# Kernel optimization log

Hardware: AMD Instinct MI355X
Metric: run time of the kernel (lower is better)

## Reference

```python
import jax, jax.numpy as jnp
import numpy as np

HEADS = 12
ROPE_THETA = 10000.0

def _rope(t):
    # t: [B, H, N, D]; lucidrains interleaved RoPE (rotate_half over adjacent pairs)
    B, H, N, D = t.shape
    inv_freq = 1.0 / (ROPE_THETA ** (jnp.arange(0, D, 2, dtype=jnp.float32) / D))  # [D/2]
    freqs = jnp.arange(N, dtype=jnp.float32)[:, None] * inv_freq[None, :]          # [N, D/2]
    freqs = jnp.repeat(freqs, 2, axis=-1)                                          # [N, D]
    cos, sin = jnp.cos(freqs), jnp.sin(freqs)
    tp = t.reshape(B, H, N, D // 2, 2)
    rot = jnp.stack([-tp[..., 1], tp[..., 0]], axis=-1).reshape(B, H, N, D)
    return t * cos + rot * sin

def setup_inputs() -> dict:
    key = jax.random.key(0)
    k1, k2, k3 = jax.random.split(key, 3)
    dim = 768
    x = jax.random.normal(k1, (2, 2048, dim), dtype=jnp.float32)
    w_qkv = jax.random.normal(k2, (3 * dim, dim), dtype=jnp.float32) * (dim ** -0.5)
    w_proj = jax.random.normal(k3, (dim, dim), dtype=jnp.float32) * (dim ** -0.5)
    b_proj = jnp.zeros((dim,), dtype=jnp.float32)
    return {"x": x, "w_qkv": w_qkv, "w_proj": w_proj, "b_proj": b_proj}

def reference(x, w_qkv, w_proj, b_proj):
    B, N, C = x.shape
    H = HEADS
    d = C // H
    scale = d ** -0.5
    qkv = x @ w_qkv.T                                # [B, N, 3C]
    q, k, v = jnp.split(qkv, 3, axis=-1)
    def to_heads(t):
        return t.reshape(B, N, H, d).transpose(0, 2, 1, 3)  # [B,H,N,d]
    q, k, v = map(to_heads, (q, k, v))
    q = _rope(q * scale)
    k = _rope(k)
    attn = jnp.einsum('bhid,bhjd->bhij', q, k)
    attn = jax.nn.softmax(attn, axis=-1)
    out = jnp.einsum('bhij,bhjd->bhid', attn, v)
    out = out.transpose(0, 2, 1, 3).reshape(B, N, C)
    return out @ w_proj.T + b_proj
```

## Files before the change

kernel.cpp:

```cpp
#include <hip/hip_runtime.h>
#include <math.h>

#define NSEQ 2048
#define CDIM 768
#define NH   12
#define HD   64
#define NB   2

typedef unsigned short u16;
typedef __attribute__((ext_vector_type(8))) short bf16x8;
typedef __attribute__((ext_vector_type(4))) float f32x4;
typedef __attribute__((ext_vector_type(8))) float f32x8;
typedef __attribute__((ext_vector_type(4))) __bf16 bf16x4t;
typedef __attribute__((ext_vector_type(8))) __bf16 bf16x8t;

__device__ __forceinline__ u16 f2bf(float x) {
    unsigned int u = __float_as_uint(x);
    u += 0x7fffu + ((u >> 16) & 1u);
    return (u16)(u >> 16);
}

__device__ __forceinline__ uint4 pack8(float4 a, float4 b) {
    f32x8 v = {a.x, a.y, a.z, a.w, b.x, b.y, b.z, b.w};
    union { bf16x8t t; uint4 u; } o;
    o.t = __builtin_convertvector(v, bf16x8t);
    return o.u;
}

__device__ __forceinline__ float fexp2(float x) {
#if __has_builtin(__builtin_amdgcn_exp2f)
    return __builtin_amdgcn_exp2f(x);
#else
    float r; asm("v_exp_f32 %0, %1" : "=v"(r) : "v"(x)); return r;
#endif
}

#define LSTR 72
#define ESTR 136

#define GLD16(gp, lp) __builtin_amdgcn_global_load_lds( \
    (__attribute__((address_space(1))) void*)(const void*)(gp), \
    (__attribute__((address_space(3))) void*)(void*)(lp), 16, 0, 0)

__global__ __launch_bounds__(256)
void conv_kernel(const float* __restrict__ Xf, const float* __restrict__ Wqkv,
                 const float* __restrict__ Wproj, u16* __restrict__ Xb,
                 u16* __restrict__ Wqb, u16* __restrict__ Wpb)
{
    const int c = blockIdx.x * 256 + threadIdx.x;
    const float* src; u16* dst; int lc; float scl = 1.0f;
    if (c < 393216)      { src = Xf;    dst = Xb;  lc = c; }
    else if (c < 614400) { src = Wqkv;  dst = Wqb; lc = c - 393216;
                           if (lc < 73728) scl = 0.18033688011112042f; }
    else                 { src = Wproj; dst = Wpb; lc = c - 614400; }
    float4 a = *(const float4*)&src[(size_t)lc * 8];
    float4 b = *(const float4*)&src[(size_t)lc * 8 + 4];
    a.x *= scl; a.y *= scl; a.z *= scl; a.w *= scl;
    b.x *= scl; b.y *= scl; b.z *= scl; b.w *= scl;
    *(uint4*)&dst[(size_t)lc * 8] = pack8(a, b);
}

#define QKV_STAGE(BUF, kt_) do {                                              \
    _Pragma("unroll")                                                         \
    for (int it = 0; it < 4; ++it) {                                          \
        int ch = tid + 256 * it; int rr = ch >> 3;                            \
        int sc = ((ch & 7) ^ (rr & 7)) << 3;                                  \
        GLD16(Xg + (size_t)(m0 + rr) * CDIM + (kt_) + sc, &S[BUF][ch * 8]);   \
    }                                                                         \
    _Pragma("unroll")                                                         \
    for (int it = 0; it < 2; ++it) {                                          \
        int ch = tid + 256 * it; int rr = ch >> 3;                            \
        int sc = ((ch & 7) ^ (rr & 7)) << 3;                                  \
        GLD16(Wg + (size_t)(n0 + rr) * CDIM + (kt_) + sc,                     \
              &S[BUF][8192 + ch * 8]);                                        \
    }                                                                         \
} while (0)

__global__ __launch_bounds__(256)
void qkv_mfma_kernel(const u16* __restrict__ Xg, const u16* __restrict__ Wg,
                     u16* __restrict__ Qb, u16* __restrict__ Kb,
                     u16* __restrict__ Vb)
{
    __shared__ __align__(16) u16 S[2][12288];

    const int tid  = threadIdx.x;
    const int lane = tid & 63;
    const int wid  = tid >> 6;
    const int l15  = lane & 15;
    const int quad = lane >> 4;
    const int swz  = (l15 & 7) << 3;

    const int f  = blockIdx.x;
    const int xc = f & 7;
    const int s  = f >> 3;
    const int m0 = (xc * 4 + (s & 3)) * 128;
    const int n0 = (s >> 2) * 64;

    f32x4 acc[2][4];
#pragma unroll
    for (int mi = 0; mi < 2; ++mi)
#pragma unroll
        for (int ni = 0; ni < 4; ++ni)
            acc[mi][ni] = (f32x4){0.f, 0.f, 0.f, 0.f};

    QKV_STAGE(0, 0);
    __syncthreads();

    int cur = 0;
    for (int kt = 0; kt < CDIM; kt += 64) {
        if (kt + 64 < CDIM) QKV_STAGE(cur ^ 1, kt + 64);

#pragma unroll
        for (int k = 0; k < 2; ++k) {
            bf16x8 af[2];
#pragma unroll
            for (int mi = 0; mi < 2; ++mi)
                af[mi] = *(const bf16x8*)
                    &S[cur][(wid * 32 + mi * 16 + l15) * 64
                            + ((quad * 8 + 32 * k) ^ swz)];
#pragma unroll
            for (int ni = 0; ni < 4; ++ni) {
                bf16x8 bfr = *(const bf16x8*)
                    &S[cur][8192 + (ni * 16 + l15) * 64
                            + ((quad * 8 + 32 * k) ^ swz)];
#pragma unroll
                for (int mi = 0; mi < 2; ++mi)
                    acc[mi][ni] = __builtin_amdgcn_mfma_f32_16x16x32_bf16(
                        af[mi], bfr, acc[mi][ni], 0, 0, 0);
            }
        }
        __syncthreads();
        cur ^= 1;
    }

    const int bi      = m0 >> 11;
    const int tokbase = m0 & 2047;
    const int nbase   = tokbase + wid * 32;
    const int sel     = n0 / CDIM;
    const int h       = (n0 % CDIM) >> 6;
    u16* Sf = &S[0][0];

    if (sel == 2) {
        u16* Ew = Sf;
#pragma unroll
        for (int ni = 0; ni < 4; ++ni)
#pragma unroll
            for (int mi = 0; mi < 2; ++mi)
#pragma unroll
                for (int r = 0; r < 4; ++r)
                    Ew[(ni * 16 + l15) * ESTR + wid * 32 + mi * 16 + quad * 4 + r]
                        = f2bf(acc[mi][ni][r]);
        __syncthreads();
        u16* dst = Vb + (size_t)(bi * NH + h) * HD * NSEQ;
#pragma unroll
        for (int it = 0; it < 4; ++it) {
            int idx = tid + 256 * it;
            int dd  = idx >> 4;
            int c8  = (idx & 15) << 3;
            *(uint4*)&dst[(size_t)dd * NSEQ + tokbase + c8] =
                *(const uint4*)&Ew[dd * ESTR + c8];
        }
    } else {
        u16* dst = ((sel == 0) ? Qb : Kb) + (size_t)(bi * NH + h) * NSEQ * HD;
        u16* Ew = Sf + wid * 32 * LSTR;
#pragma unroll
        for (int ni = 0; ni < 4; ++ni) {
            int dd = ni * 16 + l15;
            float invf = expf(-0.14391156831212787f * (float)(dd & ~1));
#pragma unroll
            for (int mi = 0; mi < 2; ++mi) {
                f32x4 val = acc[mi][ni];
#pragma unroll
                for (int r = 0; r < 4; ++r) {
                    float e = val[r];
                    float p = __shfl_xor(e, 1);
                    int n = nbase + mi * 16 + quad * 4 + r;
                    float sv, cv;
                    __sincosf((float)n * invf, &sv, &cv);
                    float o = (dd & 1) ? (e * cv + p * sv)
                                       : (e * cv - p * sv);
                    Ew[(mi * 16 + quad * 4 + r) * LSTR + dd] = f2bf(o);
                }
            }
        }
#pragma unroll
        for (int it = 0; it < 4; ++it) {
            int ch  = lane + 64 * it;
            int tr  = ch >> 3;
            int gc8 = (ch & 7) << 3;
            *(uint4*)&dst[(size_t)(nbase + tr) * HD + gc8] =
                *(const uint4*)&Ew[tr * LSTR + gc8];
        }
    }
}

#define STAGE_KV(BUF, kt_) do {                                               \
    GLD16(Kg + ((size_t)(((kt_) << 6) + r0) * HD + cs),                       \
          &Ks[BUF][wid * 512]);                                               \
    GLD16(Kg + ((size_t)(((kt_) << 6) + r0 + 32) * HD + cs),                  \
          &Ks[BUF][wid * 512 + 2048]);                                        \
    GLD16(Vg + ((size_t)r0 * NSEQ + ((kt_) << 6) + cs),                       \
          &Vs[BUF][wid * 512]);                                               \
    GLD16(Vg + ((size_t)(r0 + 32) * NSEQ + ((kt_) << 6) + cs),                \
          &Vs[BUF][wid * 512 + 2048]);                                        \
} while (0)

#define ATTN_STEP(kt_, CUR, NXT) do {                                         \
    if ((kt_) + 1 < NSEQ / 64) STAGE_KV(NXT, (kt_) + 1);                      \
    f32x4 sacc[4];                                                            \
    _Pragma("unroll")                                                         \
    for (int mt = 0; mt < 4; ++mt) sacc[mt] = (f32x4){0.f, 0.f, 0.f, 0.f};    \
    __builtin_amdgcn_s_setprio(1);                                            \
    _Pragma("unroll")                                                         \
    for (int k = 0; k < 2; ++k) {                                             \
        _Pragma("unroll")                                                     \
        for (int mt = 0; mt < 4; ++mt) {                                      \
            bf16x8 ak = *(const bf16x8*)                                      \
                &Ks[CUR][(mt * 16 + l15) * 64 + ((quad * 8 + 32 * k) ^ swz)]; \
            sacc[mt] = __builtin_amdgcn_mfma_f32_16x16x32_bf16(               \
                ak, aq[k], sacc[mt], 0, 0, 0);                                \
        }                                                                     \
    }                                                                         \
    __builtin_amdgcn_s_setprio(0);                                            \
    _Pragma("unroll")                                                         \
    for (int mt = 0; mt < 4; ++mt) {                                          \
        f32x4 ev;                                                             \
        _Pragma("unroll")                                                     \
        for (int r = 0; r < 4; ++r) ev[r] = fexp2(sacc[mt][r]);               \
        bf16x4t pbk = __builtin_convertvector(ev, bf16x4t);                   \
        *(bf16x4t*)&Pw[l15 * 64 + ((mt * 16 + quad * 4) ^ swz)] = pbk;        \
    }                                                                         \
    __builtin_amdgcn_s_setprio(1);                                            \
    _Pragma("unroll")                                                         \
    for (int k = 0; k < 2; ++k) {                                             \
        bf16x8 ap = *(const bf16x8*)                                          \
            &Pw[l15 * 64 + ((quad * 8 + 32 * k) ^ swz)];                      \
        lacc = __builtin_amdgcn_mfma_f32_16x16x32_bf16(                       \
            ap, vone, lacc, 0, 0, 0);                                         \
        _Pragma("unroll")                                                     \
        for (int t = 0; t < 4; ++t) {                                         \
            bf16x8 bv = *(const bf16x8*)                                      \
                &Vs[CUR][(t * 16 + l15) * 64 + ((quad * 8 + 32 * k) ^ swz)];  \
            O[t] = __builtin_amdgcn_mfma_f32_16x16x32_bf16(                   \
                ap, bv, O[t], 0, 0, 0);                                       \
        }                                                                     \
    }                                                                         \
    __builtin_amdgcn_s_setprio(0);                                            \
    __syncthreads();                                                          \
} while (0)

__global__ __launch_bounds__(256)
void attn_kernel(const u16* __restrict__ Qb, const u16* __restrict__ Kb,
                 const u16* __restrict__ Vt, u16* __restrict__ AO)
{
    __shared__ __align__(16) u16 Ks[2][64 * 64];
    __shared__ __align__(16) u16 Vs[2][64 * 64];
    __shared__ __align__(16) u16 Ps[4][16 * 64];

    const int tid  = threadIdx.x;
    const int lane = tid & 63;
    const int wid  = tid >> 6;
    const int l15  = lane & 15;
    const int quad = lane >> 4;
    const int swz  = (l15 & 7) << 3;

    const int f  = blockIdx.x;
    const int i  = f >> 3;
    const int bh = (f & 7) * 3 + (i >> 5);
    const int qt = i & 31;

    const u16* Qg = Qb + ((size_t)bh * NSEQ + qt * 64) * HD;
    const u16* Kg = Kb + (size_t)bh * NSEQ * HD;
    const u16* Vg = Vt + (size_t)bh * HD * NSEQ;

    const int r0 = tid >> 3;
    const int cs = ((tid & 7) ^ (r0 & 7)) << 3;

    bf16x8 aq[2];
    aq[0] = *(const bf16x8*)&Qg[(wid * 16 + l15) * HD + quad * 8];
    aq[1] = *(const bf16x8*)&Qg[(wid * 16 + l15) * HD + quad * 8 + 32];

    union { u16 s[8]; bf16x8 v; } oneu;
#pragma unroll
    for (int ii = 0; ii < 8; ++ii) oneu.s[ii] = 0x3f80;
    const bf16x8 vone = oneu.v;

    f32x4 O[4];
#pragma unroll
    for (int t = 0; t < 4; ++t) O[t] = (f32x4){0.f, 0.f, 0.f, 0.f};
    f32x4 lacc = (f32x4){0.f, 0.f, 0.f, 0.f};

    u16* Pw = Ps[wid];

    STAGE_KV(0, 0);
    __syncthreads();

    for (int kt = 0; kt < NSEQ / 64; kt += 2) {
        ATTN_STEP(kt, 0, 1);
        ATTN_STEP(kt + 1, 1, 0);
    }

    float inv4[4];
#pragma unroll
    for (int r = 0; r < 4; ++r) inv4[r] = 1.0f / lacc[r];

    const int b = bh / NH, h = bh % NH;
#pragma unroll
    for (int r = 0; r < 4; ++r) {
        size_t orow = (size_t)b * NSEQ + qt * 64 + wid * 16 + quad * 4 + r;
#pragma unroll
        for (int t = 0; t < 4; ++t)
            AO[orow * CDIM + h * HD + t * 16 + l15] = f2bf(O[t][r] * inv4[r]);
    }
}

#define PROJ_STAGE(BUF, kt_) do {                                             \
    _Pragma("unroll")                                                         \
    for (int it = 0; it < 2; ++it) {                                          \
        int ch = tid + 256 * it; int rr = ch >> 3;                            \
        int sc = ((ch & 7) ^ (rr & 7)) << 3;                                  \
        GLD16(Ag + (size_t)(m0 + rr) * CDIM + (kt_) + sc, &S[BUF][ch * 8]);   \
        GLD16(Wg + (size_t)(n0 + rr) * CDIM + (kt_) + sc,                     \
              &S[BUF][4096 + ch * 8]);                                        \
    }                                                                         \
} while (0)

__global__ __launch_bounds__(256)
void proj_kernel(const u16* __restrict__ Ag, const u16* __restrict__ Wg,
                 const float* __restrict__ bias, float* __restrict__ out)
{
    __shared__ __align__(16) u16 S[2][8192];
    const int tid  = threadIdx.x;
    const int lane = tid & 63;
    const int wid  = tid >> 6;
    const int l15  = lane & 15;
    const int quad = lane >> 4;
    const int swz  = (l15 & 7) << 3;
    const int wr = wid >> 1, wc = wid & 1;

    const int f  = blockIdx.x;
    const int xc = f & 7;
    const int s  = f >> 3;
    const int m0 = (xc * 8 + (s & 7)) * 64;
    const int n0 = (s >> 3) * 64;

    f32x4 acc[2][2];
#pragma unroll
    for (int mi = 0; mi < 2; ++mi)
#pragma unroll
        for (int ni = 0; ni < 2; ++ni)
            acc[mi][ni] = (f32x4){0.f, 0.f, 0.f, 0.f};

    PROJ_STAGE(0, 0);
    __syncthreads();

    int cur = 0;
    for (int kt = 0; kt < CDIM; kt += 64) {
        if (kt + 64 < CDIM) PROJ_STAGE(cur ^ 1, kt + 64);

#pragma unroll
        for (int k = 0; k < 2; ++k) {
            bf16x8 af[2], bf[2];
#pragma unroll
            for (int mi = 0; mi < 2; ++mi)
                af[mi] = *(const bf16x8*)
                    &S[cur][(wr * 32 + mi * 16 + l15) * 64
                            + ((quad * 8 + 32 * k) ^ swz)];
#pragma unroll
            for (int ni = 0; ni < 2; ++ni)
                bf[ni] = *(const bf16x8*)
                    &S[cur][4096 + (wc * 32 + ni * 16 + l15) * 64
                            + ((quad * 8 + 32 * k) ^ swz)];
#pragma unroll
            for (int mi = 0; mi < 2; ++mi)
#pragma unroll
                for (int ni = 0; ni < 2; ++ni)
                    acc[mi][ni] = __builtin_amdgcn_mfma_f32_16x16x32_bf16(
                        af[mi], bf[ni], acc[mi][ni], 0, 0, 0);
        }
        __syncthreads();
        cur ^= 1;
    }

#pragma unroll
    for (int ni = 0; ni < 2; ++ni) {
        int col = n0 + wc * 32 + ni * 16 + l15;
        float bb = bias[col];
#pragma unroll
        for (int mi = 0; mi < 2; ++mi) {
            int rw = m0 + wr * 32 + mi * 16 + quad * 4;
#pragma unroll
            for (int r = 0; r < 4; ++r)
                out[(size_t)(rw + r) * CDIM + col] = acc[mi][ni][r] + bb;
        }
    }
}

extern "C" void kernel_launch(void* const* d_in, const int* in_sizes, int n_in,
                              void* d_out, int out_size, void* d_ws,
                              size_t ws_size, hipStream_t stream)
{
    const float* X     = (const float*)d_in[0];
    const float* Wqkv  = (const float*)d_in[1];
    const float* Wproj = (const float*)d_in[2];
    const float* bias  = (const float*)d_in[3];
    float* out = (float*)d_out;

    const size_t per_buf = (size_t)NB * NH * NSEQ * HD;
    u16* Qb  = (u16*)d_ws;
    u16* Kb  = Qb + per_buf;
    u16* Vb  = Kb + per_buf;
    u16* XAO = Vb + per_buf;
    u16* Wqb = XAO + per_buf;
    u16* Wpb = Wqb + (size_t)3 * CDIM * CDIM;

    conv_kernel<<<dim3(2688), 256, 0, stream>>>(X, Wqkv, Wproj, XAO, Wqb, Wpb);
    qkv_mfma_kernel<<<dim3(1152), 256, 0, stream>>>(XAO, Wqb, Qb, Kb, Vb);
    attn_kernel<<<dim3(768), 256, 0, stream>>>(Qb, Kb, Vb, XAO);
    proj_kernel<<<dim3(768), 256, 0, stream>>>(XAO, Wpb, bias, out);
}
```

Baseline: 144.8 us.

## Switch attention to 32x32x16 MFMA with split-KV warps and register-shuffled P

New measurement: 147.5 us. No clear change (+1.9%).

```diff
diff --git a/kernel.cpp b/kernel.cpp
--- a/kernel.cpp
+++ b/kernel.cpp
@@ -11,6 +11,9 @@
 typedef __attribute__((ext_vector_type(8))) short bf16x8;
 typedef __attribute__((ext_vector_type(4))) float f32x4;
 typedef __attribute__((ext_vector_type(8))) float f32x8;
+typedef __attribute__((ext_vector_type(16))) float f32x16;
+typedef __attribute__((ext_vector_type(2))) float f32x2;
+typedef __attribute__((ext_vector_type(2))) __bf16 bf16x2t;
 typedef __attribute__((ext_vector_type(4))) __bf16 bf16x4t;
 typedef __attribute__((ext_vector_type(8))) __bf16 bf16x8t;
 
@@ -24,6 +27,12 @@
     f32x8 v = {a.x, a.y, a.z, a.w, b.x, b.y, b.z, b.w};
     union { bf16x8t t; uint4 u; } o;
     o.t = __builtin_convertvector(v, bf16x8t);
+    return o.u;
+}
+
+__device__ __forceinline__ unsigned cvtpk(float lo, float hi) {
+    union { bf16x2t t; unsigned u; } o;
+    o.t = __builtin_convertvector((f32x2){lo, hi}, bf16x2t);
     return o.u;
 }
 
@@ -195,57 +204,55 @@
 }
 
 #define STAGE_KV(BUF, kt_) do {                                               \
-    GLD16(Kg + ((size_t)(((kt_) << 6) + r0) * HD + cs),                       \
-          &Ks[BUF][wid * 512]);                                               \
-    GLD16(Kg + ((size_t)(((kt_) << 6) + r0 + 32) * HD + cs),                  \
-          &Ks[BUF][wid * 512 + 2048]);                                        \
-    GLD16(Vg + ((size_t)r0 * NSEQ + ((kt_) << 6) + cs),                       \
-          &Vs[BUF][wid * 512]);                                               \
-    GLD16(Vg + ((size_t)(r0 + 32) * NSEQ + ((kt_) << 6) + cs),                \
-          &Vs[BUF][wid * 512 + 2048]);                                        \
+    _Pragma("unroll")                                                         \
+    for (int j_ = 0; j_ < 2; ++j_) {                                          \
+        int c0_ = wid * 128 + j_ * 64;                                        \
+        int rr  = (c0_ + lane) >> 3;                                          \
+        int sc  = ((lane & 7) ^ (rr & 7)) << 3;                               \
+        GLD16(Kg + ((size_t)(((kt_) << 6) + rr) * HD + sc),                   \
+              &Ks[BUF][c0_ * 8]);                                             \
+        GLD16(Vg + ((size_t)rr * NSEQ + ((kt_) << 6) + sc),                   \
+              &Vs[BUF][c0_ * 8]);                                             \
+    }                                                                         \
 } while (0)
 
 #define ATTN_STEP(kt_, CUR, NXT) do {                                         \
     if ((kt_) + 1 < NSEQ / 64) STAGE_KV(NXT, (kt_) + 1);                      \
-    f32x4 sacc[4];                                                            \
-    _Pragma("unroll")                                                         \
-    for (int mt = 0; mt < 4; ++mt) sacc[mt] = (f32x4){0.f, 0.f, 0.f, 0.f};    \
+    f32x16 s0 = {};                                                           \
     __builtin_amdgcn_s_setprio(1);                                            \
     _Pragma("unroll")                                                         \
-    for (int k = 0; k < 2; ++k) {                                             \
-        _Pragma("unroll")                                                     \
-        for (int mt = 0; mt < 4; ++mt) {                                      \
-            bf16x8 ak = *(const bf16x8*)                                      \
-                &Ks[CUR][(mt * 16 + l15) * 64 + ((quad * 8 + 32 * k) ^ swz)]; \
-            sacc[mt] = __builtin_amdgcn_mfma_f32_16x16x32_bf16(               \
-                ak, aq[k], sacc[mt], 0, 0, 0);                                \
-        }                                                                     \
+    for (int s = 0; s < 4; ++s) {                                             \
+        bf16x8 ak = *(const bf16x8*)                                          \
+            &Ks[CUR][(wk * 32 + l31) * 64 + ((16 * s + 8 * hi) ^ swz)];       \
+        s0 = __builtin_amdgcn_mfma_f32_32x32x16_bf16(ak, bq[s], s0, 0, 0, 0); \
     }                                                                         \
     __builtin_amdgcn_s_setprio(0);                                            \
     _Pragma("unroll")                                                         \
-    for (int mt = 0; mt < 4; ++mt) {                                          \
-        f32x4 ev;                                                             \
-        _Pragma("unroll")                                                     \
-        for (int r = 0; r < 4; ++r) ev[r] = fexp2(sacc[mt][r]);               \
-        bf16x4t pbk = __builtin_convertvector(ev, bf16x4t);                   \
-        *(bf16x4t*)&Pw[l15 * 64 + ((mt * 16 + quad * 4) ^ swz)] = pbk;        \
-    }                                                                         \
-    __builtin_amdgcn_s_setprio(1);                                            \
-    _Pragma("unroll")                                                         \
-    for (int k = 0; k < 2; ++k) {                                             \
-        bf16x8 ap = *(const bf16x8*)                                          \
-            &Pw[l15 * 64 + ((quad * 8 + 32 * k) ^ swz)];                      \
-        lacc = __builtin_amdgcn_mfma_f32_16x16x32_bf16(                       \
-            ap, vone, lacc, 0, 0, 0);                                         \
-        _Pragma("unroll")                                                     \
-        for (int t = 0; t < 4; ++t) {                                         \
-            bf16x8 bv = *(const bf16x8*)                                      \
-                &Vs[CUR][(t * 16 + l15) * 64 + ((quad * 8 + 32 * k) ^ swz)];  \
-            O[t] = __builtin_amdgcn_mfma_f32_16x16x32_bf16(                   \
-                ap, bv, O[t], 0, 0, 0);                                       \
-        }                                                                     \
-    }                                                                         \
-    __builtin_amdgcn_s_setprio(0);                                            \
+    for (int r = 0; r < 16; ++r) s0[r] = fexp2(s0[r]);                        \
+    _Pragma("unroll")                                                         \
+    for (int t = 0; t < 2; ++t) {                                             \
+        const int sl = 8 * t;                                                 \
+        unsigned w0 = cvtpk(s0[sl + 0], s0[sl + 1]);                          \
+        unsigned w1 = cvtpk(s0[sl + 2], s0[sl + 3]);                          \
+        unsigned w2 = cvtpk(s0[sl + 4], s0[sl + 5]);                          \
+        unsigned w3 = cvtpk(s0[sl + 6], s0[sl + 7]);                          \
+        unsigned x0 = (unsigned)__shfl_xor((int)w0, 32);                      \
+        unsigned x1 = (unsigned)__shfl_xor((int)w1, 32);                      \
+        unsigned x2 = (unsigned)__shfl_xor((int)w2, 32);                      \
+        unsigned x3 = (unsigned)__shfl_xor((int)w3, 32);                      \
+        union { unsigned w[4]; bf16x8 v; } ap;                                \
+        ap.w[0] = hi ? x2 : w0;  ap.w[1] = hi ? x3 : w1;                      \
+        ap.w[2] = hi ? w2 : x0;  ap.w[3] = hi ? w3 : x1;                      \
+        const int vc = (wk * 32 + 16 * t + 8 * hi) ^ swz;                     \
+        bf16x8 bv0 = *(const bf16x8*)&Vs[CUR][l31 * 64 + vc];                 \
+        bf16x8 bv1 = *(const bf16x8*)&Vs[CUR][(32 + l31) * 64 + vc];          \
+        __builtin_amdgcn_s_setprio(1);                                        \
+        lacc = __builtin_amdgcn_mfma_f32_32x32x16_bf16(ap.v, vone, lacc,      \
+                                                       0, 0, 0);              \
+        O0 = __builtin_amdgcn_mfma_f32_32x32x16_bf16(ap.v, bv0, O0, 0, 0, 0); \
+        O1 = __builtin_amdgcn_mfma_f32_32x32x16_bf16(ap.v, bv1, O1, 0, 0, 0); \
+        __builtin_amdgcn_s_setprio(0);                                        \
+    }                                                                         \
     __syncthreads();                                                          \
 } while (0)
 
@@ -255,14 +262,15 @@
 {
     __shared__ __align__(16) u16 Ks[2][64 * 64];
     __shared__ __align__(16) u16 Vs[2][64 * 64];
-    __shared__ __align__(16) u16 Ps[4][16 * 64];
 
     const int tid  = threadIdx.x;
     const int lane = tid & 63;
     const int wid  = tid >> 6;
-    const int l15  = lane & 15;
-    const int quad = lane >> 4;
-    const int swz  = (l15 & 7) << 3;
+    const int wq   = wid >> 1;
+    const int wk   = wid & 1;
+    const int l31  = lane & 31;
+    const int hi   = lane >> 5;
+    const int swz  = (l31 & 7) << 3;
 
     const int f  = blockIdx.x;
     const int i  = f >> 3;
@@ -273,24 +281,18 @@
     const u16* Kg = Kb + (size_t)bh * NSEQ * HD;
     const u16* Vg = Vt + (size_t)bh * HD * NSEQ;
 
-    const int r0 = tid >> 3;
-    const int cs = ((tid & 7) ^ (r0 & 7)) << 3;
-
-    bf16x8 aq[2];
-    aq[0] = *(const bf16x8*)&Qg[(wid * 16 + l15) * HD + quad * 8];
-    aq[1] = *(const bf16x8*)&Qg[(wid * 16 + l15) * HD + quad * 8 + 32];
+    bf16x8 bq[4];
+#pragma unroll
+    for (int s = 0; s < 4; ++s)
+        bq[s] = *(const bf16x8*)&Qg[(wq * 32 + l31) * HD + 16 * s + 8 * hi];
 
     union { u16 s[8]; bf16x8 v; } oneu;
 #pragma unroll
     for (int ii = 0; ii < 8; ++ii) oneu.s[ii] = 0x3f80;
     const bf16x8 vone = oneu.v;
 
-    f32x4 O[4];
-#pragma unroll
-    for (int t = 0; t < 4; ++t) O[t] = (f32x4){0.f, 0.f, 0.f, 0.f};
-    f32x4 lacc = (f32x4){0.f, 0.f, 0.f, 0.f};
-
-    u16* Pw = Ps[wid];
+    f32x16 O0 = {}, O1 = {};
+    f32x16 lacc = {};
 
     STAGE_KV(0, 0);
     __syncthreads();
@@ -300,17 +302,33 @@
         ATTN_STEP(kt + 1, 1, 0);
     }
 
-    float inv4[4];
-#pragma unroll
-    for (int r = 0; r < 4; ++r) inv4[r] = 1.0f / lacc[r];
-
-    const int b = bh / NH, h = bh % NH;
-#pragma unroll
-    for (int r = 0; r < 4; ++r) {
-        size_t orow = (size_t)b * NSEQ + qt * 64 + wid * 16 + quad * 4 + r;
-#pragma unroll
-        for (int t = 0; t < 4; ++t)
-            AO[orow * CDIM + h * HD + t * 16 + l15] = f2bf(O[t][r] * inv4[r]);
+    float* CB = (wq == 0) ? (float*)&Ks[0][0] : (float*)&Vs[0][0];
+    if (wk == 1) {
+#pragma unroll
+        for (int r = 0; r < 16; ++r) {
+            CB[r * 64 + lane]        = O0[r];
+            CB[1024 + r * 64 + lane] = O1[r];
+            CB[2048 + r * 64 + lane] = lacc[r];
+        }
+    }
+    __syncthreads();
+    if (wk == 0) {
+#pragma unroll
+        for (int r = 0; r < 16; ++r) {
+            O0[r]   += CB[r * 64 + lane];
+            O1[r]   += CB[1024 + r * 64 + lane];
+            lacc[r] += CB[2048 + r * 64 + lane];
+        }
+        const int b = bh / NH, h = bh % NH;
+        const size_t base = ((size_t)b * NSEQ + qt * 64 + wq * 32) * CDIM
+                            + h * HD;
+#pragma unroll
+        for (int r = 0; r < 16; ++r) {
+            const int q = (r & 3) + 8 * (r >> 2) + 4 * hi;
+            const float iv = 1.0f / lacc[r];
+            AO[base + (size_t)q * CDIM + l31]      = f2bf(O0[r] * iv);
+            AO[base + (size_t)q * CDIM + 32 + l31] = f2bf(O1[r] * iv);
+        }
     }
 }
 
```

## Split attention waves into 2x2 query/key grid with cross-wave reduction

Applied to the files above, without the earlier changes.

Measured after the change: 158.2 us. 1.09x slower.

```diff
diff --git a/kernel.cpp b/kernel.cpp
--- a/kernel.cpp
+++ b/kernel.cpp
@@ -37,6 +37,7 @@
 
 #define LSTR 72
 #define ESTR 136
+#define PSTR 72
 
 #define GLD16(gp, lp) __builtin_amdgcn_global_load_lds( \
     (__attribute__((address_space(1))) void*)(const void*)(gp), \
@@ -207,42 +208,57 @@
 
 #define ATTN_STEP(kt_, CUR, NXT) do {                                         \
     if ((kt_) + 1 < NSEQ / 64) STAGE_KV(NXT, (kt_) + 1);                      \
-    f32x4 sacc[4];                                                            \
-    _Pragma("unroll")                                                         \
-    for (int mt = 0; mt < 4; ++mt) sacc[mt] = (f32x4){0.f, 0.f, 0.f, 0.f};    \
+    f32x4 sacc[2][2];                                                         \
+    _Pragma("unroll")                                                         \
+    for (int g = 0; g < 2; ++g)                                               \
+        _Pragma("unroll")                                                     \
+        for (int mt = 0; mt < 2; ++mt)                                        \
+            sacc[g][mt] = (f32x4){0.f, 0.f, 0.f, 0.f};                        \
     __builtin_amdgcn_s_setprio(1);                                            \
     _Pragma("unroll")                                                         \
     for (int k = 0; k < 2; ++k) {                                             \
         _Pragma("unroll")                                                     \
-        for (int mt = 0; mt < 4; ++mt) {                                      \
+        for (int mt = 0; mt < 2; ++mt) {                                      \
             bf16x8 ak = *(const bf16x8*)                                      \
-                &Ks[CUR][(mt * 16 + l15) * 64 + ((quad * 8 + 32 * k) ^ swz)]; \
-            sacc[mt] = __builtin_amdgcn_mfma_f32_16x16x32_bf16(               \
-                ak, aq[k], sacc[mt], 0, 0, 0);                                \
+                &Ks[CUR][(wk * 32 + mt * 16 + l15) * 64                       \
+                         + ((quad * 8 + 32 * k) ^ swz)];                      \
+            sacc[0][mt] = __builtin_amdgcn_mfma_f32_16x16x32_bf16(            \
+                ak, aq[0][k], sacc[0][mt], 0, 0, 0);                          \
+            sacc[1][mt] = __builtin_amdgcn_mfma_f32_16x16x32_bf16(            \
+                ak, aq[1][k], sacc[1][mt], 0, 0, 0);                          \
         }                                                                     \
     }                                                                         \
     __builtin_amdgcn_s_setprio(0);                                            \
     _Pragma("unroll")                                                         \
-    for (int mt = 0; mt < 4; ++mt) {                                          \
-        f32x4 ev;                                                             \
+    for (int g = 0; g < 2; ++g)                                               \
         _Pragma("unroll")                                                     \
-        for (int r = 0; r < 4; ++r) ev[r] = fexp2(sacc[mt][r]);               \
-        bf16x4t pbk = __builtin_convertvector(ev, bf16x4t);                   \
-        *(bf16x4t*)&Pw[l15 * 64 + ((mt * 16 + quad * 4) ^ swz)] = pbk;        \
-    }                                                                         \
+        for (int mt = 0; mt < 2; ++mt) {                                      \
+            f32x4 ev;                                                         \
+            _Pragma("unroll")                                                 \
+            for (int r = 0; r < 4; ++r) ev[r] = fexp2(sacc[g][mt][r]);        \
+            bf16x4t pbk = __builtin_convertvector(ev, bf16x4t);               \
+            *(bf16x4t*)&Pw[l15 * PSTR + g * 32                                \
+                           + ((mt * 16 + quad * 4) ^ pswz)] = pbk;            \
+        }                                                                     \
     __builtin_amdgcn_s_setprio(1);                                            \
-    _Pragma("unroll")                                                         \
-    for (int k = 0; k < 2; ++k) {                                             \
-        bf16x8 ap = *(const bf16x8*)                                          \
-            &Pw[l15 * 64 + ((quad * 8 + 32 * k) ^ swz)];                      \
-        lacc = __builtin_amdgcn_mfma_f32_16x16x32_bf16(                       \
-            ap, vone, lacc, 0, 0, 0);                                         \
+    {                                                                         \
+        bf16x8 ap0 = *(const bf16x8*)                                         \
+            &Pw[l15 * PSTR + ((quad * 8) ^ pswz)];                            \
+        bf16x8 ap1 = *(const bf16x8*)                                         \
+            &Pw[l15 * PSTR + 32 + ((quad * 8) ^ pswz)];                       \
+        lacc[0] = __builtin_amdgcn_mfma_f32_16x16x32_bf16(                    \
+            ap0, vone, lacc[0], 0, 0, 0);                                     \
+        lacc[1] = __builtin_amdgcn_mfma_f32_16x16x32_bf16(                    \
+            ap1, vone, lacc[1], 0, 0, 0);                                     \
         _Pragma("unroll")                                                     \
         for (int t = 0; t < 4; ++t) {                                         \
             bf16x8 bv = *(const bf16x8*)                                      \
-                &Vs[CUR][(t * 16 + l15) * 64 + ((quad * 8 + 32 * k) ^ swz)];  \
-            O[t] = __builtin_amdgcn_mfma_f32_16x16x32_bf16(                   \
-                ap, bv, O[t], 0, 0, 0);                                       \
+                &Vs[CUR][(t * 16 + l15) * 64                                  \
+                         + ((wk * 32 + quad * 8) ^ swz)];                     \
+            O[0][t] = __builtin_amdgcn_mfma_f32_16x16x32_bf16(                \
+                ap0, bv, O[0][t], 0, 0, 0);                                   \
+            O[1][t] = __builtin_amdgcn_mfma_f32_16x16x32_bf16(                \
+                ap1, bv, O[1][t], 0, 0, 0);                                   \
         }                                                                     \
     }                                                                         \
     __builtin_amdgcn_s_setprio(0);                                            \
@@ -255,14 +271,17 @@
 {
     __shared__ __align__(16) u16 Ks[2][64 * 64];
     __shared__ __align__(16) u16 Vs[2][64 * 64];
-    __shared__ __align__(16) u16 Ps[4][16 * 64];
+    __shared__ __align__(16) u16 Ps[4][16 * PSTR];
 
     const int tid  = threadIdx.x;
     const int lane = tid & 63;
     const int wid  = tid >> 6;
+    const int wq   = wid >> 1;
+    const int wk   = wid & 1;
     const int l15  = lane & 15;
     const int quad = lane >> 4;
     const int swz  = (l15 & 7) << 3;
+    const int pswz = (l15 & 3) << 3;
 
     const int f  = blockIdx.x;
     const int i  = f >> 3;
@@ -276,19 +295,27 @@
     const int r0 = tid >> 3;
     const int cs = ((tid & 7) ^ (r0 & 7)) << 3;
 
-    bf16x8 aq[2];
-    aq[0] = *(const bf16x8*)&Qg[(wid * 16 + l15) * HD + quad * 8];
-    aq[1] = *(const bf16x8*)&Qg[(wid * 16 + l15) * HD + quad * 8 + 32];
+    bf16x8 aq[2][2];
+#pragma unroll
+    for (int g = 0; g < 2; ++g)
+#pragma unroll
+        for (int k = 0; k < 2; ++k)
+            aq[g][k] = *(const bf16x8*)
+                &Qg[(wq * 32 + g * 16 + l15) * HD + quad * 8 + 32 * k];
 
     union { u16 s[8]; bf16x8 v; } oneu;
 #pragma unroll
     for (int ii = 0; ii < 8; ++ii) oneu.s[ii] = 0x3f80;
     const bf16x8 vone = oneu.v;
 
-    f32x4 O[4];
-#pragma unroll
-    for (int t = 0; t < 4; ++t) O[t] = (f32x4){0.f, 0.f, 0.f, 0.f};
-    f32x4 lacc = (f32x4){0.f, 0.f, 0.f, 0.f};
+    f32x4 O[2][4];
+#pragma unroll
+    for (int g = 0; g < 2; ++g)
+#pragma unroll
+        for (int t = 0; t < 4; ++t) O[g][t] = (f32x4){0.f, 0.f, 0.f, 0.f};
+    f32x4 lacc[2];
+    lacc[0] = (f32x4){0.f, 0.f, 0.f, 0.f};
+    lacc[1] = (f32x4){0.f, 0.f, 0.f, 0.f};
 
     u16* Pw = Ps[wid];
 
@@ -300,17 +327,37 @@
         ATTN_STEP(kt + 1, 1, 0);
     }
 
-    float inv4[4];
-#pragma unroll
-    for (int r = 0; r < 4; ++r) inv4[r] = 1.0f / lacc[r];
-
-    const int b = bh / NH, h = bh % NH;
-#pragma unroll
-    for (int r = 0; r < 4; ++r) {
-        size_t orow = (size_t)b * NSEQ + qt * 64 + wid * 16 + quad * 4 + r;
-#pragma unroll
-        for (int t = 0; t < 4; ++t)
-            AO[orow * CDIM + h * HD + t * 16 + l15] = f2bf(O[t][r] * inv4[r]);
+    f32x4* CB = (wq == 0) ? (f32x4*)&Ks[0][0] : (f32x4*)&Vs[0][0];
+    if (wk == 1) {
+#pragma unroll
+        for (int g = 0; g < 2; ++g) {
+#pragma unroll
+            for (int t = 0; t < 4; ++t)
+                CB[(g * 4 + t) * 64 + lane] = O[g][t];
+            CB[512 + g * 64 + lane] = lacc[g];
+        }
+    }
+    __syncthreads();
+    if (wk == 0) {
+        const int b = bh / NH, h = bh % NH;
+#pragma unroll
+        for (int g = 0; g < 2; ++g) {
+            f32x4 lsum = lacc[g] + CB[512 + g * 64 + lane];
+            float inv4[4];
+#pragma unroll
+            for (int r = 0; r < 4; ++r) inv4[r] = 1.0f / lsum[r];
+#pragma unroll
+            for (int t = 0; t < 4; ++t) {
+                f32x4 o = O[g][t] + CB[(g * 4 + t) * 64 + lane];
+#pragma unroll
+                for (int r = 0; r < 4; ++r) {
+                    size_t orow = (size_t)b * NSEQ + qt * 64 + wq * 32
+                                  + g * 16 + quad * 4 + r;
+                    AO[orow * CDIM + h * HD + t * 16 + l15] =
+                        f2bf(o[r] * inv4[r]);
+                }
+            }
+        }
     }
 }
 
```
